# Optimization experiments

Hardware: AMD Instinct MI355X
Metric: run time of the kernel (lower is better)

## Reference

```python
import jax, jax.numpy as jnp
import numpy as np

N_PEDS = 4096
TOPK = 4  # init n


def setup_inputs() -> dict:
    key = jax.random.key(0)
    k1, k2, k3, k4 = jax.random.split(key, 4)
    obs1 = jax.random.normal(k1, (N_PEDS, 2), dtype=jnp.float32)
    obs2 = jax.random.normal(k2, (N_PEDS, 2), dtype=jnp.float32)
    # torch.nn.Linear(6, 8): W [8,6], b [8]
    W = jax.random.normal(k3, (8, 6), dtype=jnp.float32) * (1.0 / np.sqrt(6.0))
    b = jax.random.normal(k4, (8,), dtype=jnp.float32) * 0.01
    return {"obs1": obs1, "obs2": obs2, "W": W, "b": b}


def reference(obs1, obs2, W, b):
    n = obs2.shape[0]
    k = TOPK
    vel = obs2 - obs1                                   # [n,2]
    # rel_vel[i,j] = vel[j] - vel[i]; rel_pos[i,j] = obs2[j] - obs2[i]
    rel_vel = vel[None, :, :] - vel[:, None, :]          # [n,n,2]
    rel_pos = obs2[None, :, :] - obs2[:, None, :]        # [n,n,2]
    # original norm includes the visible tag (=1): sqrt(dx^2+dy^2+1);
    # squared distance is order-equivalent for top-k.
    dist2 = rel_pos[..., 0] ** 2 + rel_pos[..., 1] ** 2 + 1.0
    eye = jnp.eye(n, dtype=bool)
    dist2 = jnp.where(eye, jnp.inf, dist2)               # exclude self
    _, idx = jax.lax.top_k(-dist2, k)                    # k smallest dists, [n,k]
    pos_k = jnp.take_along_axis(rel_pos, idx[:, :, None], axis=1)  # [n,k,2]
    vel_k = jnp.take_along_axis(rel_vel, idx[:, :, None], axis=1)  # [n,k,2]
    tag = jnp.ones((n, k, 1), dtype=pos_k.dtype)
    feat = jnp.concatenate([pos_k, tag, vel_k, tag], axis=-1)      # [n,k,6]
    emb = jax.nn.relu(jnp.einsum('nkd,od->nko', feat, W) + b)      # [n,k,8]
    return emb.reshape(n, -1)                                      # [n,32]
```

## Files before the change

kernel.cpp:

```cpp
#include <hip/hip_runtime.h>
#include <stdint.h>

#define N_PEDS 4096

__device__ __forceinline__ unsigned long long u64min(unsigned long long a, unsigned long long b) {
    return a < b ? a : b;
}
__device__ __forceinline__ unsigned long long u64max(unsigned long long a, unsigned long long b) {
    return a < b ? b : a;
}

__global__ __launch_bounds__(256) void nn_tag_pool_kernel(
    const float* __restrict__ obs1, const float* __restrict__ obs2,
    const float* __restrict__ W, const float* __restrict__ b,
    float* __restrict__ out)
{
    __shared__ __align__(16) float2 pos[N_PEDS];
    __shared__ float sW[48];
    __shared__ float sB[8];

    const int tid = threadIdx.x;

    {
        const float4* src = (const float4*)obs2;
        float4* dst = (float4*)pos;
        #pragma unroll
        for (int k = 0; k < 8; ++k) {
            dst[tid + k * 256] = src[tid + k * 256];
        }
    }
    if (tid < 48) sW[tid] = W[tid];
    if (tid < 8)  sB[tid] = b[tid];
    __syncthreads();

    const int wave = tid >> 6;
    const int lane = tid & 63;
    const int i = blockIdx.x * 4 + wave;

    const float2 pi = pos[i];
    const float xi = pi.x, yi = pi.y;

    unsigned long long t0 = ~0ull, t1 = ~0ull, t2 = ~0ull, t3 = ~0ull;

    #pragma unroll 4
    for (int j = lane; j < N_PEDS; j += 64) {
        float2 pj = pos[j];
        float dx = __fsub_rn(pj.x, xi);
        float dy = __fsub_rn(pj.y, yi);
        float d  = __fadd_rn(__fadd_rn(__fmul_rn(dx, dx), __fmul_rn(dy, dy)), 1.0f);
        unsigned long long key =
            ((unsigned long long)__float_as_uint(d) << 32) | (unsigned)j;
        if (j == i) key = ~0ull;
        t3 = u64min(t3, u64max(t2, key));
        t2 = u64min(t2, u64max(t1, key));
        t1 = u64min(t1, u64max(t0, key));
        t0 = u64min(t0, key);
    }

    #pragma unroll
    for (int m = 1; m < 64; m <<= 1) {
        unsigned long long b0 = __shfl_xor(t0, m, 64);
        unsigned long long b1 = __shfl_xor(t1, m, 64);
        unsigned long long b2 = __shfl_xor(t2, m, 64);
        unsigned long long b3 = __shfl_xor(t3, m, 64);
        unsigned long long e0 = u64min(t0, b3);
        unsigned long long e1 = u64min(t1, b2);
        unsigned long long e2 = u64min(t2, b1);
        unsigned long long e3 = u64min(t3, b0);
        unsigned long long f0 = u64min(e0, e2), f2 = u64max(e0, e2);
        unsigned long long f1 = u64min(e1, e3), f3 = u64max(e1, e3);
        t0 = u64min(f0, f1); t1 = u64max(f0, f1);
        t2 = u64min(f2, f3); t3 = u64max(f2, f3);
    }

    if (lane < 32) {
        const int k = lane >> 3;
        const int o = lane & 7;
        unsigned long long tk = (k == 0) ? t0 : (k == 1) ? t1 : (k == 2) ? t2 : t3;
        const int j = (int)(unsigned)(tk & 0xFFFFFFFFu);

        float2 pj = pos[j];
        float px = pj.x - xi;
        float py = pj.y - yi;
        float o1jx = obs1[2 * j],     o1jy = obs1[2 * j + 1];
        float o1ix = obs1[2 * i],     o1iy = obs1[2 * i + 1];
        float vx = (pj.x - o1jx) - (xi - o1ix);
        float vy = (pj.y - o1jy) - (yi - o1iy);

        const float* w = &sW[o * 6];
        float acc = sB[o] + w[0] * px + w[1] * py + w[2]
                          + w[3] * vx + w[4] * vy + w[5];
        out[i * 32 + k * 8 + o] = acc > 0.0f ? acc : 0.0f;
    }
}

extern "C" void kernel_launch(void* const* d_in, const int* in_sizes, int n_in,
                              void* d_out, int out_size, void* d_ws, size_t ws_size,
                              hipStream_t stream) {
    const float* obs1 = (const float*)d_in[0];
    const float* obs2 = (const float*)d_in[1];
    const float* W    = (const float*)d_in[2];
    const float* b    = (const float*)d_in[3];
    float* out        = (float*)d_out;

    hipLaunchKernelGGL(nn_tag_pool_kernel, dim3(N_PEDS / 4), dim3(256), 0, stream,
                       obs1, obs2, W, b, out);
}
```

Before: 76.79 us.

## Insert candidate pairs into top-4 via merge network and use 512-thread blocks

Each lane now reads a float4 of two positions per iteration, sorts the two keys, and merges the pair into its running top-4 with a small compare-exchange network. This replaces two separate four-step insertions and halves the LDS load count and loop iterations. Blocks grow to 512 threads (8 rows each) with launch bounds requesting 4 blocks per CU, so each block's obs2 copy into shared memory serves twice as many rows. The lane-to-index mapping changes, so each lane's candidates become interleaved pairs, and the larger block raises register and shared memory pressure per block.

```diff
diff --git a/kernel.cpp b/kernel.cpp
--- a/kernel.cpp
+++ b/kernel.cpp
@@ -2,15 +2,17 @@
 #include <stdint.h>
 
 #define N_PEDS 4096
+typedef unsigned long long u64;
 
-__device__ __forceinline__ unsigned long long u64min(unsigned long long a, unsigned long long b) {
-    return a < b ? a : b;
-}
-__device__ __forceinline__ unsigned long long u64max(unsigned long long a, unsigned long long b) {
-    return a < b ? b : a;
+__device__ __forceinline__ u64 u64min(u64 a, u64 b) { return a < b ? a : b; }
+__device__ __forceinline__ u64 u64max(u64 a, u64 b) { return a < b ? b : a; }
+__device__ __forceinline__ void ce(u64& a, u64& b) {
+    u64 lo = u64min(a, b);
+    b = u64max(a, b);
+    a = lo;
 }
 
-__global__ __launch_bounds__(256) void nn_tag_pool_kernel(
+__global__ __launch_bounds__(512, 4) void nn_tag_pool_kernel(
     const float* __restrict__ obs1, const float* __restrict__ obs2,
     const float* __restrict__ W, const float* __restrict__ b,
     float* __restrict__ out)
@@ -25,9 +27,7 @@
         const float4* src = (const float4*)obs2;
         float4* dst = (float4*)pos;
         #pragma unroll
-        for (int k = 0; k < 8; ++k) {
-            dst[tid + k * 256] = src[tid + k * 256];
-        }
+        for (int k = 0; k < 4; ++k) dst[tid + k * 512] = src[tid + k * 512];
     }
     if (tid < 48) sW[tid] = W[tid];
     if (tid < 8)  sB[tid] = b[tid];
@@ -35,40 +35,51 @@
 
     const int wave = tid >> 6;
     const int lane = tid & 63;
-    const int i = blockIdx.x * 4 + wave;
+    const int i = blockIdx.x * 8 + wave;
 
     const float2 pi = pos[i];
     const float xi = pi.x, yi = pi.y;
+    const float INF = __int_as_float(0x7f800000);
 
-    unsigned long long t0 = ~0ull, t1 = ~0ull, t2 = ~0ull, t3 = ~0ull;
+    u64 t0 = ~0ull, t1 = ~0ull, t2 = ~0ull, t3 = ~0ull;
+
+    const float4* pos4 = (const float4*)pos;
 
     #pragma unroll 4
-    for (int j = lane; j < N_PEDS; j += 64) {
-        float2 pj = pos[j];
-        float dx = __fsub_rn(pj.x, xi);
-        float dy = __fsub_rn(pj.y, yi);
-        float d  = __fadd_rn(__fadd_rn(__fmul_rn(dx, dx), __fmul_rn(dy, dy)), 1.0f);
-        unsigned long long key =
-            ((unsigned long long)__float_as_uint(d) << 32) | (unsigned)j;
-        if (j == i) key = ~0ull;
-        t3 = u64min(t3, u64max(t2, key));
-        t2 = u64min(t2, u64max(t1, key));
-        t1 = u64min(t1, u64max(t0, key));
-        t0 = u64min(t0, key);
+    for (int it = 0; it < 32; ++it) {
+        const int j2 = lane + (it << 6);
+        float4 p = pos4[j2];
+        const int c0 = j2 * 2, c1 = c0 + 1;
+
+        float dx0 = __fsub_rn(p.x, xi), dy0 = __fsub_rn(p.y, yi);
+        float d0  = __fadd_rn(__fadd_rn(__fmul_rn(dx0, dx0), __fmul_rn(dy0, dy0)), 1.0f);
+        float dx1 = __fsub_rn(p.z, xi), dy1 = __fsub_rn(p.w, yi);
+        float d1  = __fadd_rn(__fadd_rn(__fmul_rn(dx1, dx1), __fmul_rn(dy1, dy1)), 1.0f);
+        if (c0 == i) d0 = INF;
+        if (c1 == i) d1 = INF;
+
+        u64 ka = ((u64)__float_as_uint(d0) << 32) | (unsigned)c0;
+        u64 kb = ((u64)__float_as_uint(d1) << 32) | (unsigned)c1;
+
+        ce(ka, kb);
+        u64 m2 = u64min(t2, kb);
+        u64 m3 = u64min(t3, ka);
+        ce(t0, m2); ce(t1, m3); ce(t0, t1); ce(m2, m3);
+        t2 = m2; t3 = m3;
     }
 
     #pragma unroll
     for (int m = 1; m < 64; m <<= 1) {
-        unsigned long long b0 = __shfl_xor(t0, m, 64);
-        unsigned long long b1 = __shfl_xor(t1, m, 64);
-        unsigned long long b2 = __shfl_xor(t2, m, 64);
-        unsigned long long b3 = __shfl_xor(t3, m, 64);
-        unsigned long long e0 = u64min(t0, b3);
-        unsigned long long e1 = u64min(t1, b2);
-        unsigned long long e2 = u64min(t2, b1);
-        unsigned long long e3 = u64min(t3, b0);
-        unsigned long long f0 = u64min(e0, e2), f2 = u64max(e0, e2);
-        unsigned long long f1 = u64min(e1, e3), f3 = u64max(e1, e3);
+        u64 b0 = __shfl_xor(t0, m, 64);
+        u64 b1 = __shfl_xor(t1, m, 64);
+        u64 b2 = __shfl_xor(t2, m, 64);
+        u64 b3 = __shfl_xor(t3, m, 64);
+        u64 e0 = u64min(t0, b3);
+        u64 e1 = u64min(t1, b2);
+        u64 e2 = u64min(t2, b1);
+        u64 e3 = u64min(t3, b0);
+        u64 f0 = u64min(e0, e2), f2 = u64max(e0, e2);
+        u64 f1 = u64min(e1, e3), f3 = u64max(e1, e3);
         t0 = u64min(f0, f1); t1 = u64max(f0, f1);
         t2 = u64min(f2, f3); t3 = u64max(f2, f3);
     }
@@ -76,14 +87,14 @@
     if (lane < 32) {
         const int k = lane >> 3;
         const int o = lane & 7;
-        unsigned long long tk = (k == 0) ? t0 : (k == 1) ? t1 : (k == 2) ? t2 : t3;
+        u64 tk = (k == 0) ? t0 : (k == 1) ? t1 : (k == 2) ? t2 : t3;
         const int j = (int)(unsigned)(tk & 0xFFFFFFFFu);
 
         float2 pj = pos[j];
         float px = pj.x - xi;
         float py = pj.y - yi;
-        float o1jx = obs1[2 * j],     o1jy = obs1[2 * j + 1];
-        float o1ix = obs1[2 * i],     o1iy = obs1[2 * i + 1];
+        float o1jx = obs1[2 * j], o1jy = obs1[2 * j + 1];
+        float o1ix = obs1[2 * i], o1iy = obs1[2 * i + 1];
         float vx = (pj.x - o1jx) - (xi - o1ix);
         float vy = (pj.y - o1jy) - (yi - o1iy);
 
@@ -103,6 +114,6 @@
     const float* b    = (const float*)d_in[3];
     float* out        = (float*)d_out;
 
-    hipLaunchKernelGGL(nn_tag_pool_kernel, dim3(N_PEDS / 4), dim3(256), 0, stream,
+    hipLaunchKernelGGL(nn_tag_pool_kernel, dim3(N_PEDS / 8), dim3(512), 0, stream,
                        obs1, obs2, W, b, out);
 }
```

New measurement: 75.09 us. -2.2%, faster.
